# Performance work log

Hardware: AMD Instinct MI355X
Metric: run time of the kernel (lower is better)

Reference implementation:

```python
import jax, jax.numpy as jnp
import numpy as np

B, K, M, D = 2048, 64, 64, 256
NI, EPS, MI = 15, 0.05, 3


def setup_inputs() -> dict:
    key = jax.random.key(0)
    ks = jax.random.split(key, 8)
    sq = jax.random.normal(ks[0], (B, K, D), dtype=jnp.float32)
    sr = jax.random.normal(ks[1], (B, M, D), dtype=jnp.float32)
    mq = jax.random.uniform(ks[2], (B, K), dtype=jnp.float32)
    mr = jax.random.uniform(ks[3], (B, M), dtype=jnp.float32)
    scale = 1.0 / np.sqrt(D)
    W1 = jax.random.normal(ks[4], (D, D), dtype=jnp.float32) * scale
    b1 = jnp.zeros((D,), dtype=jnp.float32)
    W2 = jax.random.normal(ks[5], (D, D), dtype=jnp.float32) * scale
    b2 = jnp.zeros((D,), dtype=jnp.float32)
    return {"sq": sq, "sr": sr, "mq": mq, "mr": mr,
            "W1": W1, "b1": b1, "W2": W2, "b2": b2}


def _mlp(x, W1, b1, W2, b2):
    # nn.Linear: x @ W.T + b
    h = jax.nn.relu(jnp.einsum('bnd,ed->bne', x, W1) + b1)
    return jnp.einsum('bnd,ed->bne', h, W2) + b2


def _cdist(x, y):
    # Euclidean pairwise distance [B,K,M]
    x2 = jnp.sum(x * x, -1)[:, :, None]
    y2 = jnp.sum(y * y, -1)[:, None, :]
    xy = jnp.einsum('bkd,bmd->bkm', x, y)
    return jnp.sqrt(jnp.clip(x2 + y2 - 2.0 * xy, 0.0))


def reference(sq, sr, mq, mr, W1, b1, W2, b2):
    fq = _mlp(sq, W1, b1, W2, b2)
    fr = _mlp(sr, W1, b1, W2, b2)
    C = _cdist(fq, fr)                                   # [B,K,M]
    lK = (-C / EPS
          + jnp.log(jnp.clip(mq, 1e-8))[:, :, None]
          + jnp.log(jnp.clip(mr, 1e-8))[:, None, :])

    la0 = jnp.zeros((B, K, 1), dtype=C.dtype)
    lb0 = jnp.zeros((B, 1, M), dtype=C.dtype)

    def sink_body(_, carry):
        la, lb = carry
        la = -jax.nn.logsumexp(lK + lb, axis=2, keepdims=True)
        lb = -jax.nn.logsumexp(lK + la, axis=1, keepdims=True)
        return (la, lb)

    la, lb = jax.lax.fori_loop(0, NI, sink_body, (la0, lb0))
    T = jnp.exp(lK + la + lb)

    def pow_body(_, T):
        T = T * T
        T = T / (jnp.sum(T, -1, keepdims=True) + 1e-8)
        T = T / (jnp.sum(T, -2, keepdims=True) + 1e-8)
        return T

    T = jax.lax.fori_loop(0, MI, pow_body, T)
    c = jnp.sum(T * C, axis=(-1, -2))                    # [B]
    return (jax.nn.sigmoid(-c), T, C, c)
```

## Files before the change

### kernel.cpp

```cpp
#include <hip/hip_runtime.h>
#include <math.h>

#define NB    2048
#define KK    64
#define MM    64
#define DD    256
#define NITER 15
#define MITER 3
#define IEPS  20.0f

typedef __bf16 bf16_t;
typedef bf16_t bf16x8 __attribute__((ext_vector_type(8)));
typedef bf16_t bf16x4 __attribute__((ext_vector_type(4)));
typedef float  f32x16 __attribute__((ext_vector_type(16)));

#define XSTR 264
#define CSTR 65


__global__ __launch_bounds__(256) void convert_w_frag(const float* __restrict__ W1,
                                                      const float* __restrict__ W2,
                                                      bf16_t* __restrict__ wf) {
    const int j19 = blockIdx.x * 256 + threadIdx.x;
    const int layer = j19 >> 16;
    const int j = j19 & 65535;
    const int u    = j & 7;
    const int lane = (j >> 3) & 63;
    const int kc   = (j >> 9) & 15;
    const int eb   = j >> 13;
    const int l31  = lane & 31;
    const int lh   = lane >> 5;
    const int src  = (eb * 32 + l31) * 256 + kc * 16 + lh * 8 + u;
    wf[j19] = (bf16_t)(layer ? W2[src] : W1[src]);
}

__global__ __launch_bounds__(512, 4) void sinkhorn_all(
    const float* __restrict__ sq, const float* __restrict__ sr,
    const float* __restrict__ mq, const float* __restrict__ mr,
    const float* __restrict__ b1, const float* __restrict__ b2,
    const bf16_t* __restrict__ wf,
    float* __restrict__ out) {

    __shared__ __align__(16) char smem[128 * XSTR * 2];
    bf16_t* Xs = (bf16_t*)smem;
    float*  Cs = (float*)smem;
    float*  Ts = (float*)(smem + 64 * CSTR * 4);
    __shared__ float nrm[128];
    __shared__ float lmq_s[64], lmr_s[64], la_s[64], lb_s[64];
    __shared__ float b1_s[256], b2_s[256];
    __shared__ float red_s[8];

    const int b  = blockIdx.x;
    const int t  = threadIdx.x;
    const int ln = t & 63;
    const int wv = t >> 6;
    const int l31 = ln & 31;
    const int lh  = ln >> 5;

    {
        const float4* sq4 = (const float4*)(sq + (size_t)b * 64 * 256);
        const float4* sr4 = (const float4*)(sr + (size_t)b * 64 * 256);
        float4 xr[16];
        #pragma unroll
        for (int it = 0; it < 16; ++it) {
            const int r = wv + it * 8;
            xr[it] = (r < 64) ? sq4[r * 64 + ln] : sr4[(r - 64) * 64 + ln];
        }
        #pragma unroll
        for (int it = 0; it < 16; ++it) {
            const int r = wv + it * 8;
            bf16x4 p;
            p[0] = (bf16_t)xr[it].x; p[1] = (bf16_t)xr[it].y;
            p[2] = (bf16_t)xr[it].z; p[3] = (bf16_t)xr[it].w;
            *(bf16x4*)&Xs[(size_t)r * XSTR + ln * 4] = p;
        }
        if (t < 256) b1_s[t] = b1[t];
        else         b2_s[t - 256] = b2[t - 256];
        if (t >= 256) {
            const int u = t - 256;
            if (u < 64)        lmq_s[u]       = __logf(fmaxf(mq[(size_t)b * 64 + u], 1e-8f));
            else if (u < 128)  lmr_s[u - 64]  = __logf(fmaxf(mr[(size_t)b * 64 + (u - 64)], 1e-8f));
            else if (u < 192)  lb_s[u - 128]  = 0.0f;
        }
    }
    __syncthreads();

    bf16x4 hreg[2][2][4];
    {
        const bf16_t* wbase = wf + ((size_t)wv * 16) * 512 + ln * 8;
        f32x16 acc[2][2];
        #pragma unroll
        for (int i = 0; i < 16; ++i) {
            acc[0][0][i] = 0.0f; acc[0][1][i] = 0.0f;
            acc[1][0][i] = 0.0f; acc[1][1][i] = 0.0f;
        }
        #pragma unroll
        for (int kg = 0; kg < 2; ++kg) {
            bf16x8 af[8];
            #pragma unroll
            for (int u = 0; u < 8; ++u)
                af[u] = *(const bf16x8*)(wbase + (size_t)(kg * 8 + u) * 512);
            #pragma unroll
            for (int half = 0; half < 2; ++half) {
                const bf16_t* x0 = Xs + (size_t)(half * 64 + l31) * XSTR + lh * 8;
                const bf16_t* x1 = x0 + 32 * XSTR;
                #pragma unroll
                for (int u = 0; u < 8; ++u) {
                    const int kc = kg * 8 + u;
                    bf16x8 bx0 = *(const bf16x8*)(x0 + kc * 16);
                    bf16x8 bx1 = *(const bf16x8*)(x1 + kc * 16);
                    acc[half][0] = __builtin_amdgcn_mfma_f32_32x32x16_bf16(af[u], bx0, acc[half][0], 0, 0, 0);
                    acc[half][1] = __builtin_amdgcn_mfma_f32_32x32x16_bf16(af[u], bx1, acc[half][1], 0, 0, 0);
                }
            }
        }
        const int e0 = wv * 32;
        #pragma unroll
        for (int half = 0; half < 2; ++half)
            #pragma unroll
            for (int z = 0; z < 2; ++z)
                #pragma unroll
                for (int g = 0; g < 4; ++g) {
                    const int e = e0 + 8 * g + 4 * lh;
                    #pragma unroll
                    for (int rr = 0; rr < 4; ++rr) {
                        float v = acc[half][z][4 * g + rr] + b1_s[e + rr];
                        hreg[half][z][g][rr] = (bf16_t)fmaxf(v, 0.0f);
                    }
                }
    }
    __syncthreads();

    {
        const int e0 = wv * 32;
        #pragma unroll
        for (int half = 0; half < 2; ++half)
            #pragma unroll
            for (int z = 0; z < 2; ++z) {
                const int n = half * 64 + z * 32 + l31;
                #pragma unroll
                for (int g = 0; g < 4; ++g)
                    *(bf16x4*)&Xs[(size_t)n * XSTR + e0 + 8 * g + 4 * lh] = hreg[half][z][g];
            }
    }
    __syncthreads();

    {
        const bf16_t* wbase = wf + 65536 + ((size_t)wv * 16) * 512 + ln * 8;
        f32x16 acc[2][2];
        #pragma unroll
        for (int i = 0; i < 16; ++i) {
            acc[0][0][i] = 0.0f; acc[0][1][i] = 0.0f;
            acc[1][0][i] = 0.0f; acc[1][1][i] = 0.0f;
        }
        #pragma unroll
        for (int kg = 0; kg < 2; ++kg) {
            bf16x8 af[8];
            #pragma unroll
            for (int u = 0; u < 8; ++u)
                af[u] = *(const bf16x8*)(wbase + (size_t)(kg * 8 + u) * 512);
            #pragma unroll
            for (int half = 0; half < 2; ++half) {
                const bf16_t* x0 = Xs + (size_t)(half * 64 + l31) * XSTR + lh * 8;
                const bf16_t* x1 = x0 + 32 * XSTR;
                #pragma unroll
                for (int u = 0; u < 8; ++u) {
                    const int kc = kg * 8 + u;
                    bf16x8 bx0 = *(const bf16x8*)(x0 + kc * 16);
                    bf16x8 bx1 = *(const bf16x8*)(x1 + kc * 16);
                    acc[half][0] = __builtin_amdgcn_mfma_f32_32x32x16_bf16(af[u], bx0, acc[half][0], 0, 0, 0);
                    acc[half][1] = __builtin_amdgcn_mfma_f32_32x32x16_bf16(af[u], bx1, acc[half][1], 0, 0, 0);
                }
            }
        }
        const int e0 = wv * 32;
        #pragma unroll
        for (int half = 0; half < 2; ++half)
            #pragma unroll
            for (int z = 0; z < 2; ++z)
                #pragma unroll
                for (int g = 0; g < 4; ++g) {
                    const int e = e0 + 8 * g + 4 * lh;
                    #pragma unroll
                    for (int rr = 0; rr < 4; ++rr)
                        hreg[half][z][g][rr] = (bf16_t)(acc[half][z][4 * g + rr] + b2_s[e + rr]);
                }
    }
    __syncthreads();

    {
        const int e0 = wv * 32;
        #pragma unroll
        for (int half = 0; half < 2; ++half)
            #pragma unroll
            for (int z = 0; z < 2; ++z) {
                const int n = half * 64 + z * 32 + l31;
                #pragma unroll
                for (int g = 0; g < 4; ++g)
                    *(bf16x4*)&Xs[(size_t)n * XSTR + e0 + 8 * g + 4 * lh] = hreg[half][z][g];
            }
    }
    __syncthreads();

    {
        const int r = t >> 2;
        const int q = t & 3;
        const bf16_t* frow = &Xs[(size_t)r * XSTR + q * 64];
        float s = 0.0f;
        #pragma unroll
        for (int c = 0; c < 8; ++c) {
            bf16x8 v = *(const bf16x8*)(frow + c * 8);
            #pragma unroll
            for (int u = 0; u < 8; ++u) { float f = (float)v[u]; s = fmaf(f, f, s); }
        }
        s += __shfl_xor(s, 1);
        s += __shfl_xor(s, 2);
        if (q == 0) nrm[r] = s;
    }
    __syncthreads();

    float cvv[16];
    int qbase = 0, mcol = 0;
    if (wv < 4) {
        const int qt = wv >> 1, rt = wv & 1;
        const bf16_t* qa = &Xs[(size_t)(qt * 32 + l31) * XSTR + lh * 8];
        const bf16_t* ra = &Xs[(size_t)(64 + rt * 32 + l31) * XSTR + lh * 8];
        f32x16 acc;
        #pragma unroll
        for (int i = 0; i < 16; ++i) acc[i] = 0.0f;
        #pragma unroll
        for (int kc = 0; kc < 16; ++kc) {
            bf16x8 av = *(const bf16x8*)(qa + kc * 16);
            bf16x8 bv = *(const bf16x8*)(ra + kc * 16);
            acc = __builtin_amdgcn_mfma_f32_32x32x16_bf16(av, bv, acc, 0, 0, 0);
        }
        mcol  = rt * 32 + l31;
        qbase = qt * 32;
        const float nr_m = nrm[64 + mcol];
        float* outC = out + 2048 + (size_t)2048 * 4096 + (size_t)b * 4096;
        #pragma unroll
        for (int g = 0; g < 4; ++g) {
            #pragma unroll
            for (int rr = 0; rr < 4; ++rr) {
                const int q = qbase + 8 * g + 4 * lh + rr;
                float d2 = nrm[q] + nr_m - 2.0f * acc[4 * g + rr];
                float cv = sqrtf(fmaxf(d2, 0.0f));
                cvv[4 * g + rr] = cv;
                outC[q * 64 + mcol] = cv;
            }
        }
    }
    __syncthreads();
    if (wv < 4) {
        #pragma unroll
        for (int g = 0; g < 4; ++g)
            #pragma unroll
            for (int rr = 0; rr < 4; ++rr)
                Cs[(qbase + 8 * g + 4 * lh + rr) * CSTR + mcol] = cvv[4 * g + rr];
    }
    __syncthreads();

    const int ki = t >> 3;
    const int jj = t & 7;
    float rowV[8], colV[8];
    #pragma unroll
    for (int i = 0; i < 8; ++i) {
        const int m2 = jj * 8 + i;
        rowV[i] = fmaf(Cs[ki * CSTR + m2], -IEPS, lmr_s[m2]);
        colV[i] = fmaf(Cs[m2 * CSTR + ki], -IEPS, lmq_s[m2]);
    }
    const float lmq_k = lmq_s[ki];
    const float lmr_m = lmr_s[ki];

    for (int it = 0; it < NITER; ++it) {
        float mx = -1e30f;
        #pragma unroll
        for (int i = 0; i < 8; ++i) mx = fmaxf(mx, rowV[i] + lb_s[jj * 8 + i]);
        mx = fmaxf(mx, __shfl_xor(mx, 1));
        mx = fmaxf(mx, __shfl_xor(mx, 2));
        mx = fmaxf(mx, __shfl_xor(mx, 4));
        float s = 0.0f;
        #pragma unroll
        for (int i = 0; i < 8; ++i) s += __expf(rowV[i] + lb_s[jj * 8 + i] - mx);
        s += __shfl_xor(s, 1);
        s += __shfl_xor(s, 2);
        s += __shfl_xor(s, 4);
        if (jj == 0) la_s[ki] = -(lmq_k + mx + __logf(s));
        __syncthreads();

        mx = -1e30f;
        #pragma unroll
        for (int i = 0; i < 8; ++i) mx = fmaxf(mx, colV[i] + la_s[jj * 8 + i]);
        mx = fmaxf(mx, __shfl_xor(mx, 1));
        mx = fmaxf(mx, __shfl_xor(mx, 2));
        mx = fmaxf(mx, __shfl_xor(mx, 4));
        float s2 = 0.0f;
        #pragma unroll
        for (int i = 0; i < 8; ++i) s2 += __expf(colV[i] + la_s[jj * 8 + i] - mx);
        s2 += __shfl_xor(s2, 1);
        s2 += __shfl_xor(s2, 2);
        s2 += __shfl_xor(s2, 4);
        if (jj == 0) lb_s[ki] = -(lmr_m + mx + __logf(s2));
        __syncthreads();
    }

    {
        const float base = lmq_k + la_s[ki];
        #pragma unroll
        for (int i = 0; i < 8; ++i) {
            const int m2 = jj * 8 + i;
            Ts[ki * CSTR + m2] = __expf(rowV[i] + lb_s[m2] + base);
        }
    }
    __syncthreads();

    for (int pi = 0; pi < MITER; ++pi) {
        float vv[8], rs = 0.0f;
        #pragma unroll
        for (int i = 0; i < 8; ++i) {
            float v = Ts[ki * CSTR + jj * 8 + i];
            v = v * v; vv[i] = v; rs += v;
        }
        rs += __shfl_xor(rs, 1); rs += __shfl_xor(rs, 2); rs += __shfl_xor(rs, 4);
        float inv = 1.0f / (rs + 1e-8f);
        #pragma unroll
        for (int i = 0; i < 8; ++i) Ts[ki * CSTR + jj * 8 + i] = vv[i] * inv;
        __syncthreads();

        float cs = 0.0f;
        #pragma unroll
        for (int i = 0; i < 8; ++i) { float v = Ts[(jj * 8 + i) * CSTR + ki]; vv[i] = v; cs += v; }
        cs += __shfl_xor(cs, 1); cs += __shfl_xor(cs, 2); cs += __shfl_xor(cs, 4);
        inv = 1.0f / (cs + 1e-8f);
        #pragma unroll
        for (int i = 0; i < 8; ++i) Ts[(jj * 8 + i) * CSTR + ki] = vv[i] * inv;
        __syncthreads();
    }

    {
        float part = 0.0f;
        float tq[8];
        #pragma unroll
        for (int i = 0; i < 8; ++i) {
            const int m2 = jj * 8 + i;
            float tv = Ts[ki * CSTR + m2];
            tq[i] = tv;
            part = fmaf(tv, Cs[ki * CSTR + m2], part);
        }
        float* outT = out + 2048 + (size_t)b * 4096 + ki * 64 + jj * 8;
        ((float4*)outT)[0] = make_float4(tq[0], tq[1], tq[2], tq[3]);
        ((float4*)outT)[1] = make_float4(tq[4], tq[5], tq[6], tq[7]);
        #pragma unroll
        for (int off = 1; off < 64; off <<= 1) part += __shfl_xor(part, off);
        if (ln == 0) red_s[wv] = part;
    }
    __syncthreads();
    if (t == 0) {
        float c = 0.0f;
        #pragma unroll
        for (int w = 0; w < 8; ++w) c += red_s[w];
        out[2048 + (size_t)2 * 2048 * 4096 + b] = c;
        out[b] = 1.0f / (1.0f + __expf(c));
    }
}

extern "C" void kernel_launch(void* const* d_in, const int* in_sizes, int n_in,
                              void* d_out, int out_size, void* d_ws, size_t ws_size,
                              hipStream_t stream) {
    const float* sq = (const float*)d_in[0];
    const float* sr = (const float*)d_in[1];
    const float* mq = (const float*)d_in[2];
    const float* mr = (const float*)d_in[3];
    const float* W1 = (const float*)d_in[4];
    const float* b1 = (const float*)d_in[5];
    const float* W2 = (const float*)d_in[6];
    const float* b2 = (const float*)d_in[7];

    bf16_t* wf = (bf16_t*)d_ws;

    convert_w_frag<<<512, 256, 0, stream>>>(W1, W2, wf);
    sinkhorn_all<<<NB, 512, 0, stream>>>(sq, sr, mq, mr, b1, b2, wf, (float*)d_out);
}
```

Baseline: 431.8 us.

## Split fused MLP+cdist+Sinkhorn kernel into two kernels via global C

Splits the single fused kernel into an MLP/cdist kernel that writes C to the output buffer, and a separate Sinkhorn kernel that reads C back from global memory. The Sinkhorn kernel uses a much smaller shared-memory footprint and requests higher occupancy (launch bounds 512,8), so the latency-bound iterative phase can run with more resident blocks and is no longer tied to the MLP's register and LDS usage. The cost is an extra kernel launch and a global re-read of the 32 MB C matrix.

```diff
diff --git a/kernel.cpp b/kernel.cpp
--- a/kernel.cpp
+++ b/kernel.cpp
@@ -34,21 +34,16 @@
     wf[j19] = (bf16_t)(layer ? W2[src] : W1[src]);
 }
 
-__global__ __launch_bounds__(512, 4) void sinkhorn_all(
+__global__ __launch_bounds__(512, 4) void mlp_cdist(
     const float* __restrict__ sq, const float* __restrict__ sr,
-    const float* __restrict__ mq, const float* __restrict__ mr,
     const float* __restrict__ b1, const float* __restrict__ b2,
     const bf16_t* __restrict__ wf,
     float* __restrict__ out) {
 
     __shared__ __align__(16) char smem[128 * XSTR * 2];
     bf16_t* Xs = (bf16_t*)smem;
-    float*  Cs = (float*)smem;
-    float*  Ts = (float*)(smem + 64 * CSTR * 4);
     __shared__ float nrm[128];
-    __shared__ float lmq_s[64], lmr_s[64], la_s[64], lb_s[64];
     __shared__ float b1_s[256], b2_s[256];
-    __shared__ float red_s[8];
 
     const int b  = blockIdx.x;
     const int t  = threadIdx.x;
@@ -76,12 +71,6 @@
         }
         if (t < 256) b1_s[t] = b1[t];
         else         b2_s[t - 256] = b2[t - 256];
-        if (t >= 256) {
-            const int u = t - 256;
-            if (u < 64)        lmq_s[u]       = __logf(fmaxf(mq[(size_t)b * 64 + u], 1e-8f));
-            else if (u < 128)  lmr_s[u - 64]  = __logf(fmaxf(mr[(size_t)b * 64 + (u - 64)], 1e-8f));
-            else if (u < 192)  lb_s[u - 128]  = 0.0f;
-        }
     }
     __syncthreads();
 
@@ -219,8 +208,6 @@
     }
     __syncthreads();
 
-    float cvv[16];
-    int qbase = 0, mcol = 0;
     if (wv < 4) {
         const int qt = wv >> 1, rt = wv & 1;
         const bf16_t* qa = &Xs[(size_t)(qt * 32 + l31) * XSTR + lh * 8];
@@ -234,8 +221,8 @@
             bf16x8 bv = *(const bf16x8*)(ra + kc * 16);
             acc = __builtin_amdgcn_mfma_f32_32x32x16_bf16(av, bv, acc, 0, 0, 0);
         }
-        mcol  = rt * 32 + l31;
-        qbase = qt * 32;
+        const int mcol  = rt * 32 + l31;
+        const int qbase = qt * 32;
         const float nr_m = nrm[64 + mcol];
         float* outC = out + 2048 + (size_t)2048 * 4096 + (size_t)b * 4096;
         #pragma unroll
@@ -244,30 +231,52 @@
             for (int rr = 0; rr < 4; ++rr) {
                 const int q = qbase + 8 * g + 4 * lh + rr;
                 float d2 = nrm[q] + nr_m - 2.0f * acc[4 * g + rr];
-                float cv = sqrtf(fmaxf(d2, 0.0f));
-                cvv[4 * g + rr] = cv;
-                outC[q * 64 + mcol] = cv;
-            }
-        }
-    }
-    __syncthreads();
-    if (wv < 4) {
-        #pragma unroll
-        for (int g = 0; g < 4; ++g)
-            #pragma unroll
-            for (int rr = 0; rr < 4; ++rr)
-                Cs[(qbase + 8 * g + 4 * lh + rr) * CSTR + mcol] = cvv[4 * g + rr];
-    }
-    __syncthreads();
-
+                outC[q * 64 + mcol] = sqrtf(fmaxf(d2, 0.0f));
+            }
+        }
+    }
+}
+
+__global__ __launch_bounds__(512, 8) void sinkhorn_from_C(
+    const float* __restrict__ mq, const float* __restrict__ mr,
+    float* __restrict__ out) {
+
+    __shared__ float Cs[64 * CSTR];
+    __shared__ float Ts[64 * CSTR];
+    __shared__ float lmq_s[64], lmr_s[64], la_s[64], lb_s[64];
+    __shared__ float red_s[8];
+
+    const int b  = blockIdx.x;
+    const int t  = threadIdx.x;
+    const int ln = t & 63;
+    const int wv = t >> 6;
     const int ki = t >> 3;
     const int jj = t & 7;
+
+    const float* Cg = out + 2048 + (size_t)2048 * 4096 + (size_t)b * 4096 + ki * 64 + jj * 8;
+    const float4 c0 = ((const float4*)Cg)[0];
+    const float4 c1 = ((const float4*)Cg)[1];
+
+    if (t < 64)        lmq_s[t]       = __logf(fmaxf(mq[(size_t)b * 64 + t], 1e-8f));
+    else if (t < 128)  lmr_s[t - 64]  = __logf(fmaxf(mr[(size_t)b * 64 + (t - 64)], 1e-8f));
+    else if (t < 192)  lb_s[t - 128]  = 0.0f;
+
+    {
+        float* cr = &Cs[ki * CSTR + jj * 8];
+        cr[0] = c0.x; cr[1] = c0.y; cr[2] = c0.z; cr[3] = c0.w;
+        cr[4] = c1.x; cr[5] = c1.y; cr[6] = c1.z; cr[7] = c1.w;
+    }
+    __syncthreads();
+
     float rowV[8], colV[8];
-    #pragma unroll
-    for (int i = 0; i < 8; ++i) {
-        const int m2 = jj * 8 + i;
-        rowV[i] = fmaf(Cs[ki * CSTR + m2], -IEPS, lmr_s[m2]);
-        colV[i] = fmaf(Cs[m2 * CSTR + ki], -IEPS, lmq_s[m2]);
+    {
+        const float cv[8] = {c0.x, c0.y, c0.z, c0.w, c1.x, c1.y, c1.z, c1.w};
+        #pragma unroll
+        for (int i = 0; i < 8; ++i)
+            rowV[i] = fmaf(cv[i], -IEPS, lmr_s[jj * 8 + i]);
+        #pragma unroll
+        for (int i = 0; i < 8; ++i)
+            colV[i] = fmaf(Cs[(jj * 8 + i) * CSTR + ki], -IEPS, lmq_s[jj * 8 + i]);
     }
     const float lmq_k = lmq_s[ki];
     const float lmr_m = lmr_s[ki];
@@ -379,5 +388,6 @@
     bf16_t* wf = (bf16_t*)d_ws;
 
     convert_w_frag<<<512, 256, 0, stream>>>(W1, W2, wf);
-    sinkhorn_all<<<NB, 512, 0, stream>>>(sq, sr, mq, mr, b1, b2, wf, (float*)d_out);
+    mlp_cdist<<<NB, 512, 0, stream>>>(sq, sr, b1, b2, wf, (float*)d_out);
+    sinkhorn_from_C<<<NB, 512, 0, stream>>>(mq, mr, (float*)d_out);
 }
```

Measured after the change: 419.2 us. 1.03x faster.
